# Kernel optimization log

Hardware: AMD Instinct MI355X
Metric: run time of the kernel (lower is better)

The kernel has to match this reference:

```python
import jax, jax.numpy as jnp
import numpy as np

NEG = -1e9


def setup_inputs() -> dict:
    key = jax.random.key(0)
    k1, k2, k3, k4 = jax.random.split(key, 4)
    R, N, D = 64, 200000, 256
    hs = jax.random.normal(k1, (R, D), dtype=jnp.float32)
    es = jax.random.normal(k2, (N, D), dtype=jnp.float32)
    W = jax.random.normal(k3, (D, D), dtype=jnp.float32) / np.sqrt(D)
    mask = jax.random.randint(k4, (R, N), 0, 2) > 0
    return {"hs": hs, "es": es, "W": W, "mask": mask, "n_output": 50}


def reference(hs, es, W, mask, n_output):
    # MatchingLayer: bilinear match scores[r, n] = hs_r^T W es_n  -> [R, N]
    original_scores = (hs @ W) @ es.T
    mu = original_scores.mean()
    std = original_scores.std(ddof=1)  # torch .std() is unbiased
    scores = (original_scores - mu) / std
    # logits used for expansion scores (differentiable)
    logits = jax.nn.log_softmax(scores, axis=-1) + jax.nn.log_softmax(scores, axis=0)
    # detached probabilities for selection
    d = jax.lax.stop_gradient(scores)
    row_probs = jnp.maximum(jax.nn.softmax(jnp.where(mask, d, NEG), axis=-1), 1e-6)
    col_probs = jnp.maximum(jax.nn.softmax(jnp.where(mask, d, NEG), axis=0), 1e-6)
    # deterministic (eval) path: assign each candidate to its argmax category
    index = jnp.argmax(col_probs, axis=0)  # [N]
    R = scores.shape[0]
    valid = mask & (index[None, :] == jnp.arange(R)[:, None])  # [R, N]
    sel = jnp.where(valid, row_probs, -jnp.inf)
    top_vals, top_idx = jax.lax.top_k(sel, n_output)  # [R, n_output]
    ok = jnp.isfinite(top_vals)  # rows with fewer candidates than n_output -> padded
    expansions = jnp.where(ok, top_idx, -1)  # [R, n_output], -1 = pad
    # expansion_scores[i] = logits[:, expansion_i].T -> [n_output, R]
    exp_scores = jnp.transpose(logits[:, top_idx], (1, 2, 0))  # [R, n_output, R]
    exp_scores = exp_scores * ok[:, :, None].astype(exp_scores.dtype)
    return expansions, exp_scores
```

## Files before the change

kernel.cpp:

```cpp
#include <hip/hip_runtime.h>
#include <math.h>

#define RR 64
#define DD 256
#define CAP 6144


__device__ __forceinline__ void get_mu_istd(const double* sums, int N, float& fmu, float& istd) {
  double M = (double)RR * (double)N;
  double mu = sums[0] / M;
  double var = (sums[1] - sums[0] * sums[0] / M) / (M - 1.0);
  fmu = (float)mu;
  istd = (float)(1.0 / sqrt(var));
}

__device__ __forceinline__ void cp16(const void* g, void* l) {
  __builtin_amdgcn_global_load_lds((const __attribute__((address_space(1))) void*)g,
                                   (__attribute__((address_space(3))) void*)l, 16, 0, 0);
}


__global__ __launch_bounds__(256) void k_mask(const void* __restrict__ maskp,
                                              unsigned long long* __restrict__ mbits,
                                              int N) {
  __shared__ int f;
  int tid = threadIdx.x;
  if (tid == 0) f = 0;
  __syncthreads();
  {
    const unsigned* mw = (const unsigned*)maskp;
    int mode = 0;
    for (int i = tid; i < 4096; i += 256) {
      unsigned v = mw[i];
      if (v == 0x3f800000u) mode = 2;
      else if (v > 1u && mode != 2) mode = 1;
    }
    if (mode) atomicMax(&f, mode);
  }
  __syncthreads();
  const int mode = f;

  int n = blockIdx.x * 256 + tid;
  if (n >= N) return;
  unsigned long long b = 0;
  if (mode == 1) {
    const unsigned char* m = (const unsigned char*)maskp;
#pragma unroll
    for (int r = 0; r < RR; ++r)
      b |= (unsigned long long)(m[(size_t)r * N + n] != 0) << r;
  } else if (mode == 2) {
    const float* m = (const float*)maskp;
#pragma unroll
    for (int r = 0; r < RR; ++r)
      b |= (unsigned long long)(m[(size_t)r * N + n] != 0.f) << r;
  } else {
    const int* m = (const int*)maskp;
#pragma unroll
    for (int r = 0; r < RR; ++r)
      b |= (unsigned long long)(m[(size_t)r * N + n] != 0) << r;
  }
  mbits[n] = b;
}


__global__ __launch_bounds__(256) void k_hsw(const float* __restrict__ hs,
                                             const float* __restrict__ W,
                                             float* __restrict__ hsW) {
  int i = blockIdx.x;
  int j = threadIdx.x;
  float acc = 0.f;
  for (int k = 0; k < DD; ++k) acc = fmaf(hs[i * DD + k], W[k * DD + j], acc);
  hsW[i * DD + j] = acc;
}


__global__ __launch_bounds__(256) void k_scores(const float* __restrict__ es,
                                                const float* __restrict__ hsW,
                                                const unsigned long long* __restrict__ mbits,
                                                float* __restrict__ scores,
                                                float* __restrict__ colmax,
                                                int* __restrict__ colargmax,
                                                float* __restrict__ qpart,
                                                double* __restrict__ spart,
                                                int N) {
  __shared__ float lds[20480];
  const int tid = threadIdx.x;
  const int lane = tid & 63;
  const int ty = __builtin_amdgcn_readfirstlane(tid >> 6);
  const int n0 = blockIdx.x * 256;
  const int R0 = ty * 16;
  const int nb = n0 + lane;

  const int srow = ty * 8 + (lane >> 3);
  const int sg4 = (((lane & 7) ^ ((lane >> 3) & 7)) << 2);
  const int wrow = ty * 16 + (lane >> 2);
  const int wg4 = (lane & 3) << 2;

  float4 acc[16];
#pragma unroll
  for (int i = 0; i < 16; ++i) acc[i] = make_float4(0.f, 0.f, 0.f, 0.f);

  auto stage = [&](float* ebase, float* wbase, int kc) {
#pragma unroll
    for (int p = 0; p < 8; ++p) {
      const int col = p * 32 + srow;
      const int rr = min(n0 + col, N - 1);
      cp16(es + (size_t)rr * DD + kc + sg4, ebase + p * 1024 + ty * 256);
    }
    cp16(hsW + (size_t)wrow * DD + kc + wg4, wbase + ty * 256);
    cp16(hsW + (size_t)wrow * DD + kc + 16 + wg4, wbase + 1024 + ty * 256);
  };

  stage(lds, lds + 16384, 0);
  asm volatile("s_waitcnt vmcnt(0)" ::: "memory");
  __syncthreads();

  const int swz = (lane & 7);

  for (int kc = 0; kc < DD; kc += 32) {
    const int cur = (kc >> 5) & 1;
    float* ebC = lds + (cur ? 8192 : 0);
    float* wbC = lds + 16384 + (cur ? 2048 : 0);
    if (kc + 32 < DD) {
      float* ebN = lds + (cur ? 0 : 8192);
      float* wbN = lds + 16384 + (cur ? 0 : 2048);
      stage(ebN, wbN, kc + 32);
    }
#pragma unroll
    for (int k = 0; k < 32; k += 4) {
      const int eswz = (((k >> 2) ^ swz) << 2);
      const float4 e0 = *(const float4*)(ebC + (lane       ) * 32 + eswz);
      const float4 e1 = *(const float4*)(ebC + (lane +  64 ) * 32 + eswz);
      const float4 e2 = *(const float4*)(ebC + (lane + 128 ) * 32 + eswz);
      const float4 e3 = *(const float4*)(ebC + (lane + 192 ) * 32 + eswz);
      const float* wk = wbC + ((k >> 4) * 1024) + (k & 15);
#pragma unroll
      for (int i = 0; i < 16; ++i) {
        const float4 w = *(const float4*)(wk + (R0 + i) * 16);
        acc[i].x = fmaf(w.x, e0.x, fmaf(w.y, e0.y, fmaf(w.z, e0.z, fmaf(w.w, e0.w, acc[i].x))));
        acc[i].y = fmaf(w.x, e1.x, fmaf(w.y, e1.y, fmaf(w.z, e1.z, fmaf(w.w, e1.w, acc[i].y))));
        acc[i].z = fmaf(w.x, e2.x, fmaf(w.y, e2.y, fmaf(w.z, e2.z, fmaf(w.w, e2.w, acc[i].z))));
        acc[i].w = fmaf(w.x, e3.x, fmaf(w.y, e3.y, fmaf(w.z, e3.z, fmaf(w.w, e3.w, acc[i].w))));
      }
    }
    asm volatile("s_waitcnt vmcnt(0)" ::: "memory");
    __syncthreads();
  }

  bool val[4];
#pragma unroll
  for (int c = 0; c < 4; ++c) val[c] = (nb + 64 * c) < N;

#pragma unroll
  for (int i = 0; i < 16; ++i) {
    float* dst = scores + (size_t)(R0 + i) * N + nb;
    float v[4] = {acc[i].x, acc[i].y, acc[i].z, acc[i].w};
#pragma unroll
    for (int c = 0; c < 4; ++c)
      if (val[c]) dst[64 * c] = v[c];
  }

  unsigned long long mb[4];
#pragma unroll
  for (int c = 0; c < 4; ++c) mb[c] = val[c] ? mbits[nb + 64 * c] : 0ull;

  float ps1[4], ps2[4], pcm[4], pbv[4];
  int pbr[4];
#pragma unroll
  for (int c = 0; c < 4; ++c) { ps1[c] = 0.f; ps2[c] = 0.f; pcm[c] = -INFINITY; pbv[c] = -INFINITY; pbr[c] = -1; }

#pragma unroll
  for (int i = 0; i < 16; ++i) {
    const int rrow = R0 + i;
    float v[4] = {acc[i].x, acc[i].y, acc[i].z, acc[i].w};
    float q = -INFINITY, qm = -INFINITY;
#pragma unroll
    for (int c = 0; c < 4; ++c) {
      ps1[c] += v[c];
      ps2[c] = fmaf(v[c], v[c], ps2[c]);
      pcm[c] = fmaxf(pcm[c], v[c]);
      bool bit = (mb[c] >> rrow) & 1ull;
      if (bit && (v[c] > pbv[c])) { pbv[c] = v[c]; pbr[c] = rrow; }
      float qv = val[c] ? v[c] : -INFINITY;
      q = fmaxf(q, qv);
      if (bit) qm = fmaxf(qm, qv);
    }
#pragma unroll
    for (int o = 32; o > 0; o >>= 1) {
      q = fmaxf(q, __shfl_down(q, o));
      qm = fmaxf(qm, __shfl_down(qm, o));
    }
    if (lane == 0) {
      qpart[(size_t)blockIdx.x * 128 + rrow] = q;
      qpart[(size_t)blockIdx.x * 128 + 64 + rrow] = qm;
    }
  }

  __syncthreads();
  float* Ls1 = lds;
  float* Ls2 = lds + 1024;
  float* Lcm = lds + 2048;
  float* Lbv = lds + 3072;
  int* Lbr = (int*)(lds + 4096);
  double* red = (double*)(lds + 5120);
#pragma unroll
  for (int c = 0; c < 4; ++c) {
    int col = lane + 64 * c;
    Ls1[ty * 256 + col] = ps1[c];
    Ls2[ty * 256 + col] = ps2[c];
    Lcm[ty * 256 + col] = pcm[c];
    Lbv[ty * 256 + col] = pbv[c];
    Lbr[ty * 256 + col] = pbr[c];
  }
  __syncthreads();

  const int n = n0 + tid;
  float s1 = 0.f, s2 = 0.f;
  if (n < N) {
    s1 = Ls1[tid] + Ls1[256 + tid] + Ls1[512 + tid] + Ls1[768 + tid];
    s2 = Ls2[tid] + Ls2[256 + tid] + Ls2[512 + tid] + Ls2[768 + tid];
    float cm = fmaxf(fmaxf(Lcm[tid], Lcm[256 + tid]), fmaxf(Lcm[512 + tid], Lcm[768 + tid]));
    colmax[n] = cm;
    float bv = -INFINITY;
    int br = -1;
#pragma unroll
    for (int w2 = 0; w2 < 4; ++w2) {
      float b = Lbv[w2 * 256 + tid];
      if (b > bv) { bv = b; br = Lbr[w2 * 256 + tid]; }
    }
    colargmax[n] = br;
  }

  double d1 = (double)s1, d2 = (double)s2;
#pragma unroll
  for (int o = 32; o > 0; o >>= 1) {
    d1 += __shfl_down(d1, o);
    d2 += __shfl_down(d2, o);
  }
  if ((tid & 63) == 0) { red[ty * 2] = d1; red[ty * 2 + 1] = d2; }
  __syncthreads();
  if (tid == 0) {
    spart[(size_t)blockIdx.x * 2] = red[0] + red[2] + red[4] + red[6];
    spart[(size_t)blockIdx.x * 2 + 1] = red[1] + red[3] + red[5] + red[7];
  }
}


__global__ __launch_bounds__(256) void k_redmax(const float* __restrict__ qpart,
                                                float* __restrict__ rowmaxf,
                                                int NBlk) {
  const int slot = blockIdx.x;
  const int tid = threadIdx.x, lane = tid & 63, ty = tid >> 6;
  __shared__ float w[4];
  float m = -INFINITY;
  for (int i = tid; i < NBlk; i += 256) m = fmaxf(m, qpart[(size_t)i * 128 + slot]);
#pragma unroll
  for (int o = 32; o > 0; o >>= 1) m = fmaxf(m, __shfl_down(m, o));
  if (lane == 0) w[ty] = m;
  __syncthreads();
  if (tid == 0) rowmaxf[slot] = fmaxf(fmaxf(w[0], w[1]), fmaxf(w[2], w[3]));
}


__global__ __launch_bounds__(256) void k_redsum(const double* __restrict__ spart,
                                                double* __restrict__ sums,
                                                int NBlk) {
  const int tid = threadIdx.x, lane = tid & 63, ty = tid >> 6;
  __shared__ double r[8];
  double s0 = 0.0, s1 = 0.0;
  for (int i = tid; i < NBlk; i += 256) {
    s0 += spart[(size_t)i * 2];
    s1 += spart[(size_t)i * 2 + 1];
  }
#pragma unroll
  for (int o = 32; o > 0; o >>= 1) {
    s0 += __shfl_down(s0, o);
    s1 += __shfl_down(s1, o);
  }
  if (lane == 0) { r[ty * 2] = s0; r[ty * 2 + 1] = s1; }
  __syncthreads();
  if (tid == 0) {
    sums[0] = r[0] + r[2] + r[4] + r[6];
    sums[1] = r[1] + r[3] + r[5] + r[7];
  }
}


__global__ __launch_bounds__(256) void k_colpass(const float* __restrict__ scores,
                                                 const float* __restrict__ colmax,
                                                 const int* __restrict__ colargmax,
                                                 const unsigned long long* __restrict__ mbits,
                                                 const double* __restrict__ sums,
                                                 const float* __restrict__ rowmaxf,
                                                 float* __restrict__ collse,
                                                 float* __restrict__ colpart,
                                                 int* __restrict__ cnt,
                                                 float* __restrict__ candx,
                                                 int* __restrict__ candn,
                                                 int N) {
  __shared__ float rmS[64], suS[64], smS[64];
  __shared__ float rpu[64 * 4], rpm[64 * 4];
  __shared__ int lcnt[64], lbase[64];
  const int tid = threadIdx.x, lane = tid & 63, ty = tid >> 6;
  float fmu, istd;
  get_mu_istd(sums, N, fmu, istd);
  if (tid < 64) {
    rmS[tid] = rowmaxf[tid];
    lcnt[tid] = 0;
  }
  __syncthreads();
  float gm = rmS[0];
#pragma unroll
  for (int r = 1; r < RR; ++r) gm = fmaxf(gm, rmS[r]);
  if (tid < 64) {
    suS[tid] = expf((gm - rmS[tid]) * istd);
    smS[tid] = expf((gm - rowmaxf[64 + tid]) * istd);
  }

  const int n = blockIdx.x * 256 + tid;
  const bool valid = n < N;
  const float cm = valid ? colmax[n] : 0.f;
  const int br = valid ? colargmax[n] : -1;
  const unsigned long long mbn = valid ? mbits[n] : 0ull;
  float colsum = 0.f, xbr = 0.f;

  for (int r = 0; r < RR; ++r) {
    float x = valid ? scores[(size_t)r * N + n] : 0.f;
    if (r == br) xbr = x;
    float E = valid ? expf((x - gm) * istd) : 0.f;
    colsum += E;
    float eu = E;
    float em = ((mbn >> r) & 1ull) ? E : 0.f;
#pragma unroll
    for (int o = 32; o > 0; o >>= 1) {
      eu += __shfl_down(eu, o);
      em += __shfl_down(em, o);
    }
    if (lane == 0) { rpu[r * 4 + ty] = eu; rpm[r * 4 + ty] = em; }
  }

  if (valid) collse[n] = logf(colsum) + (gm - cm) * istd;
  int lpos = 0;
  if (br >= 0) lpos = atomicAdd(&lcnt[br], 1);
  __syncthreads();
  if (tid < 64) {
    float su = (rpu[tid * 4] + rpu[tid * 4 + 1] + rpu[tid * 4 + 2] + rpu[tid * 4 + 3]) * suS[tid];
    float sm = (rpm[tid * 4] + rpm[tid * 4 + 1] + rpm[tid * 4 + 2] + rpm[tid * 4 + 3]) * smS[tid];
    colpart[(size_t)blockIdx.x * 128 + tid] = su;
    colpart[(size_t)blockIdx.x * 128 + 64 + tid] = sm;
    int c = lcnt[tid];
    lbase[tid] = c ? atomicAdd(&cnt[tid], c) : 0;
  }
  __syncthreads();
  if (br >= 0) {
    int pos = lbase[br] + lpos;
    if (pos < CAP) {
      candx[(size_t)br * CAP + pos] = xbr;
      candn[(size_t)br * CAP + pos] = n;
    }
  }
}


__global__ __launch_bounds__(256) void k_redacc(const float* __restrict__ colpart,
                                                const float* __restrict__ rowmaxf,
                                                float* __restrict__ rowstats,
                                                int NBlk) {
  const int slot = blockIdx.x;
  const int tid = threadIdx.x, lane = tid & 63, ty = tid >> 6;
  __shared__ float w[4];
  float s = 0.f;
  for (int i = tid; i < NBlk; i += 256) s += colpart[(size_t)i * 128 + slot];
#pragma unroll
  for (int o = 32; o > 0; o >>= 1) s += __shfl_down(s, o);
  if (lane == 0) w[ty] = s;
  __syncthreads();
  if (tid == 0) {
    float total = w[0] + w[1] + w[2] + w[3];
    if (slot < 64) {
      rowstats[slot] = rowmaxf[slot];
      rowstats[64 + slot] = logf(total);
    } else {
      rowstats[128 + (slot - 64)] = rowmaxf[slot];
      rowstats[192 + (slot - 64)] = total;
    }
  }
}


__global__ __launch_bounds__(512) void k_topk(const int* __restrict__ cnt,
                                              const float* __restrict__ candx,
                                              const int* __restrict__ candn,
                                              const double* __restrict__ sums,
                                              const float* __restrict__ rowstats,
                                              float* __restrict__ out,
                                              int* __restrict__ seln,
                                              int N, int NO) {
  int r = blockIdx.x, tid = threadIdx.x;
  __shared__ float sp[CAP];
  __shared__ int sn[CAP];
  __shared__ float wp[8];
  __shared__ int wn[8], wi[8];
  int c = min(cnt[r], CAP);
  float fmu, istd;
  get_mu_istd(sums, N, fmu, istd);
  const float rmm = rowstats[128 + r];
  const float lm = rowstats[192 + r];
  for (int i = tid; i < c; i += 512) {
    float xv = candx[(size_t)r * CAP + i];
    sp[i] = fmaxf(expf((xv - rmm) * istd) / lm, 1e-6f);
    sn[i] = candn[(size_t)r * CAP + i];
  }
  __syncthreads();
  for (int j = 0; j < NO; ++j) {
    float bp = -1.f;
    int bn = 0x7fffffff, bi = -1;
    for (int i = tid; i < c; i += 512) {
      float p = sp[i];
      int nn = sn[i];
      if (p > bp || (p == bp && nn < bn)) { bp = p; bn = nn; bi = i; }
    }
#pragma unroll
    for (int o = 32; o > 0; o >>= 1) {
      float p2 = __shfl_down(bp, o);
      int n2 = __shfl_down(bn, o);
      int i2 = __shfl_down(bi, o);
      if (p2 > bp || (p2 == bp && n2 < bn)) { bp = p2; bn = n2; bi = i2; }
    }
    if ((tid & 63) == 0) { wp[tid >> 6] = bp; wn[tid >> 6] = bn; wi[tid >> 6] = bi; }
    __syncthreads();
    if (tid == 0) {
      float fp2 = wp[0]; int fn2 = wn[0], fi2 = wi[0];
#pragma unroll
      for (int w2 = 1; w2 < 8; ++w2) {
        if (wp[w2] > fp2 || (wp[w2] == fp2 && wn[w2] < fn2)) { fp2 = wp[w2]; fn2 = wn[w2]; fi2 = wi[w2]; }
      }
      if (fp2 > 0.f) {
        out[r * NO + j] = (float)fn2;
        seln[r * NO + j] = fn2;
        sp[fi2] = -1.f;
      } else {
        out[r * NO + j] = -1.f;
        seln[r * NO + j] = -1;
      }
    }
    __syncthreads();
  }
}


__global__ void k_expand(const float* __restrict__ scores,
                         const double* __restrict__ sums,
                         const float* __restrict__ rowstats,
                         const float* __restrict__ colmax,
                         const float* __restrict__ collse,
                         const int* __restrict__ seln,
                         float* __restrict__ out,
                         int N, int NO) {
  int b = blockIdx.x;
  int r2 = threadIdx.x;
  int n = seln[b];
  float v = 0.f;
  if (n >= 0) {
    float fmu, istd;
    get_mu_istd(sums, N, fmu, istd);
    float x = scores[(size_t)r2 * N + n];
    float v1 = (x - rowstats[r2]) * istd - rowstats[64 + r2];
    float v2 = (x - colmax[n]) * istd - collse[n];
    v = v1 + v2;
  }
  out[RR * NO + (size_t)b * RR + r2] = v;
}


extern "C" void kernel_launch(void* const* d_in, const int* in_sizes, int n_in,
                              void* d_out, int out_size, void* d_ws, size_t ws_size,
                              hipStream_t stream) {
  const float* hs = (const float*)d_in[0];
  const float* es = (const float*)d_in[1];
  const float* W = (const float*)d_in[2];
  const void* mask = d_in[3];

  const int N = in_sizes[1] / DD;
  const int NO = out_size / (RR * (1 + RR));
  const int NB = (N + 255) / 256;

  char* ws = (char*)d_ws;
  size_t o = 0;
  float* scores = (float*)(ws + o);   o += (size_t)RR * N * 4;
  float* hsW = (float*)(ws + o);      o += RR * DD * 4;
  o = (o + 255) & ~(size_t)255;
  double* sums = (double*)(ws + o);
  int* cnt = (int*)(ws + o + 16);
  size_t zero_off = o, zero_bytes = 16 + 256;
  o += 512;
  float* rowstats = (float*)(ws + o); o += 256 * 4;
  float* rowmaxf = (float*)(ws + o);  o += 128 * 4;
  o = (o + 255) & ~(size_t)255;
  float* colmax = (float*)(ws + o);   o += (size_t)N * 4;
  int* colargmax = (int*)(ws + o);    o += (size_t)N * 4;
  float* collse = (float*)(ws + o);   o += (size_t)N * 4;
  o = (o + 255) & ~(size_t)255;
  unsigned long long* mbits = (unsigned long long*)(ws + o); o += (size_t)N * 8;
  o = (o + 255) & ~(size_t)255;
  float* candx = (float*)(ws + o);    o += (size_t)RR * CAP * 4;
  int* candn = (int*)(ws + o);        o += (size_t)RR * CAP * 4;
  int* seln = (int*)(ws + o);         o += (size_t)RR * NO * 4;
  o = (o + 255) & ~(size_t)255;
  float* qpart = (float*)(ws + o);    o += (size_t)NB * 128 * 4;
  double* spart = (double*)(ws + o);  o += (size_t)NB * 2 * 8;
  float* colpart = (float*)(ws + o);  o += (size_t)NB * 128 * 4;

  hipMemsetAsync(ws + zero_off, 0, zero_bytes, stream);

  k_mask<<<NB, 256, 0, stream>>>(mask, mbits, N);
  k_hsw<<<RR, 256, 0, stream>>>(hs, W, hsW);
  k_scores<<<NB, 256, 0, stream>>>(es, hsW, mbits, scores, colmax, colargmax,
                                   qpart, spart, N);
  k_redmax<<<128, 256, 0, stream>>>(qpart, rowmaxf, NB);
  k_redsum<<<1, 256, 0, stream>>>(spart, sums, NB);
  k_colpass<<<NB, 256, 0, stream>>>(scores, colmax, colargmax, mbits, sums, rowmaxf,
                                    collse, colpart, cnt, candx, candn, N);
  k_redacc<<<128, 256, 0, stream>>>(colpart, rowmaxf, rowstats, NB);
  k_topk<<<RR, 512, 0, stream>>>(cnt, candx, candn, sums, rowstats, (float*)d_out, seln,
                                 N, NO);
  k_expand<<<RR * NO, 64, 0, stream>>>(scores, sums, rowstats, colmax, collse, seln,
                                       (float*)d_out, N, NO);
}
```

Measured before the change: 632.7 us.

## Vectorize mask packing and colpass, fuse reductions and expand into topk

The mask-packing kernel now has each thread read 4 adjacent columns over 16 rows with vector loads and assembles 64-bit words via LDS. The column pass is restructured the same way, with float4 score loads and 4x fewer wave shuffles. The two small reduction kernels are merged into one launch that also zeroes the counters, replacing the memset. The expand kernel is folded into the top-k kernel. Together these cut launch count and uncoalesced narrow loads. The vector path assumes N is a multiple of 4 for alignment.

```diff
diff --git a/kernel.cpp b/kernel.cpp
--- a/kernel.cpp
+++ b/kernel.cpp
@@ -24,6 +24,7 @@
                                               unsigned long long* __restrict__ mbits,
                                               int N) {
   __shared__ int f;
+  __shared__ unsigned short pb[4][256];
   int tid = threadIdx.x;
   if (tid == 0) f = 0;
   __syncthreads();
@@ -40,26 +41,80 @@
   __syncthreads();
   const int mode = f;
 
-  int n = blockIdx.x * 256 + tid;
-  if (n >= N) return;
-  unsigned long long b = 0;
+  const int lane = tid & 63, ty = tid >> 6;
+  const int R0 = ty * 16;
+  const int n0 = blockIdx.x * 256;
+  const int n4 = n0 + lane * 4;
+  unsigned g0 = 0, g1 = 0, g2 = 0, g3 = 0;
+  const bool vec_ok = (n4 + 3) < N;
+
   if (mode == 1) {
     const unsigned char* m = (const unsigned char*)maskp;
-#pragma unroll
-    for (int r = 0; r < RR; ++r)
-      b |= (unsigned long long)(m[(size_t)r * N + n] != 0) << r;
+    if (vec_ok) {
+#pragma unroll
+      for (int i = 0; i < 16; ++i) {
+        uchar4 v = *(const uchar4*)(m + (size_t)(R0 + i) * N + n4);
+        g0 |= (unsigned)(v.x != 0) << i;
+        g1 |= (unsigned)(v.y != 0) << i;
+        g2 |= (unsigned)(v.z != 0) << i;
+        g3 |= (unsigned)(v.w != 0) << i;
+      }
+    } else {
+      unsigned* gp[4] = {&g0, &g1, &g2, &g3};
+      for (int c = 0; c < 4; ++c)
+        if (n4 + c < N)
+          for (int i = 0; i < 16; ++i)
+            *gp[c] |= (unsigned)(m[(size_t)(R0 + i) * N + n4 + c] != 0) << i;
+    }
   } else if (mode == 2) {
     const float* m = (const float*)maskp;
-#pragma unroll
-    for (int r = 0; r < RR; ++r)
-      b |= (unsigned long long)(m[(size_t)r * N + n] != 0.f) << r;
+    if (vec_ok) {
+#pragma unroll
+      for (int i = 0; i < 16; ++i) {
+        float4 v = *(const float4*)(m + (size_t)(R0 + i) * N + n4);
+        g0 |= (unsigned)(v.x != 0.f) << i;
+        g1 |= (unsigned)(v.y != 0.f) << i;
+        g2 |= (unsigned)(v.z != 0.f) << i;
+        g3 |= (unsigned)(v.w != 0.f) << i;
+      }
+    } else {
+      unsigned* gp[4] = {&g0, &g1, &g2, &g3};
+      for (int c = 0; c < 4; ++c)
+        if (n4 + c < N)
+          for (int i = 0; i < 16; ++i)
+            *gp[c] |= (unsigned)(m[(size_t)(R0 + i) * N + n4 + c] != 0.f) << i;
+    }
   } else {
     const int* m = (const int*)maskp;
-#pragma unroll
-    for (int r = 0; r < RR; ++r)
-      b |= (unsigned long long)(m[(size_t)r * N + n] != 0) << r;
-  }
-  mbits[n] = b;
+    if (vec_ok) {
+#pragma unroll
+      for (int i = 0; i < 16; ++i) {
+        int4 v = *(const int4*)(m + (size_t)(R0 + i) * N + n4);
+        g0 |= (unsigned)(v.x != 0) << i;
+        g1 |= (unsigned)(v.y != 0) << i;
+        g2 |= (unsigned)(v.z != 0) << i;
+        g3 |= (unsigned)(v.w != 0) << i;
+      }
+    } else {
+      unsigned* gp[4] = {&g0, &g1, &g2, &g3};
+      for (int c = 0; c < 4; ++c)
+        if (n4 + c < N)
+          for (int i = 0; i < 16; ++i)
+            *gp[c] |= (unsigned)(m[(size_t)(R0 + i) * N + n4 + c] != 0) << i;
+    }
+  }
+  pb[ty][lane * 4 + 0] = (unsigned short)g0;
+  pb[ty][lane * 4 + 1] = (unsigned short)g1;
+  pb[ty][lane * 4 + 2] = (unsigned short)g2;
+  pb[ty][lane * 4 + 3] = (unsigned short)g3;
+  __syncthreads();
+  const int n = n0 + tid;
+  if (n < N) {
+    mbits[n] = (unsigned long long)pb[0][tid] |
+               ((unsigned long long)pb[1][tid] << 16) |
+               ((unsigned long long)pb[2][tid] << 32) |
+               ((unsigned long long)pb[3][tid] << 48);
+  }
 }
 
 
@@ -246,42 +301,42 @@
 }
 
 
-__global__ __launch_bounds__(256) void k_redmax(const float* __restrict__ qpart,
-                                                float* __restrict__ rowmaxf,
-                                                int NBlk) {
-  const int slot = blockIdx.x;
+__global__ __launch_bounds__(256) void k_redfuse(const float* __restrict__ qpart,
+                                                 const double* __restrict__ spart,
+                                                 float* __restrict__ rowmaxf,
+                                                 double* __restrict__ sums,
+                                                 int* __restrict__ cnt,
+                                                 int NBlk) {
   const int tid = threadIdx.x, lane = tid & 63, ty = tid >> 6;
-  __shared__ float w[4];
-  float m = -INFINITY;
-  for (int i = tid; i < NBlk; i += 256) m = fmaxf(m, qpart[(size_t)i * 128 + slot]);
-#pragma unroll
-  for (int o = 32; o > 0; o >>= 1) m = fmaxf(m, __shfl_down(m, o));
-  if (lane == 0) w[ty] = m;
-  __syncthreads();
-  if (tid == 0) rowmaxf[slot] = fmaxf(fmaxf(w[0], w[1]), fmaxf(w[2], w[3]));
-}
-
-
-__global__ __launch_bounds__(256) void k_redsum(const double* __restrict__ spart,
-                                                double* __restrict__ sums,
-                                                int NBlk) {
-  const int tid = threadIdx.x, lane = tid & 63, ty = tid >> 6;
-  __shared__ double r[8];
-  double s0 = 0.0, s1 = 0.0;
-  for (int i = tid; i < NBlk; i += 256) {
-    s0 += spart[(size_t)i * 2];
-    s1 += spart[(size_t)i * 2 + 1];
-  }
-#pragma unroll
-  for (int o = 32; o > 0; o >>= 1) {
-    s0 += __shfl_down(s0, o);
-    s1 += __shfl_down(s1, o);
-  }
-  if (lane == 0) { r[ty * 2] = s0; r[ty * 2 + 1] = s1; }
-  __syncthreads();
-  if (tid == 0) {
-    sums[0] = r[0] + r[2] + r[4] + r[6];
-    sums[1] = r[1] + r[3] + r[5] + r[7];
+  if (blockIdx.x < 128) {
+    const int slot = blockIdx.x;
+    __shared__ float w[4];
+    float m = -INFINITY;
+    for (int i = tid; i < NBlk; i += 256) m = fmaxf(m, qpart[(size_t)i * 128 + slot]);
+#pragma unroll
+    for (int o = 32; o > 0; o >>= 1) m = fmaxf(m, __shfl_down(m, o));
+    if (lane == 0) w[ty] = m;
+    __syncthreads();
+    if (tid == 0) rowmaxf[slot] = fmaxf(fmaxf(w[0], w[1]), fmaxf(w[2], w[3]));
+  } else {
+    __shared__ double r[8];
+    double s0 = 0.0, s1 = 0.0;
+    for (int i = tid; i < NBlk; i += 256) {
+      s0 += spart[(size_t)i * 2];
+      s1 += spart[(size_t)i * 2 + 1];
+    }
+#pragma unroll
+    for (int o = 32; o > 0; o >>= 1) {
+      s0 += __shfl_down(s0, o);
+      s1 += __shfl_down(s1, o);
+    }
+    if (lane == 0) { r[ty * 2] = s0; r[ty * 2 + 1] = s1; }
+    if (tid < RR) cnt[tid] = 0;
+    __syncthreads();
+    if (tid == 0) {
+      sums[0] = r[0] + r[2] + r[4] + r[6];
+      sums[1] = r[1] + r[3] + r[5] + r[7];
+    }
   }
 }
 
@@ -299,9 +354,11 @@
                                                  int* __restrict__ candn,
                                                  int N) {
   __shared__ float rmS[64], suS[64], smS[64];
-  __shared__ float rpu[64 * 4], rpm[64 * 4];
+  __shared__ float rowU[64], rowM[64];
+  __shared__ float cpart[4][256];
   __shared__ int lcnt[64], lbase[64];
   const int tid = threadIdx.x, lane = tid & 63, ty = tid >> 6;
+  const int R0 = ty * 16;
   float fmu, istd;
   get_mu_istd(sums, N, fmu, istd);
   if (tid < 64) {
@@ -317,37 +374,58 @@
     smS[tid] = expf((gm - rowmaxf[64 + tid]) * istd);
   }
 
-  const int n = blockIdx.x * 256 + tid;
-  const bool valid = n < N;
-  const float cm = valid ? colmax[n] : 0.f;
-  const int br = valid ? colargmax[n] : -1;
-  const unsigned long long mbn = valid ? mbits[n] : 0ull;
-  float colsum = 0.f, xbr = 0.f;
-
-  for (int r = 0; r < RR; ++r) {
-    float x = valid ? scores[(size_t)r * N + n] : 0.f;
-    if (r == br) xbr = x;
-    float E = valid ? expf((x - gm) * istd) : 0.f;
-    colsum += E;
-    float eu = E;
-    float em = ((mbn >> r) & 1ull) ? E : 0.f;
+  const int n0 = blockIdx.x * 256;
+  const int n4 = n0 + lane * 4;
+  bool vc[4];
+  unsigned mbr[4];
+#pragma unroll
+  for (int c = 0; c < 4; ++c) {
+    vc[c] = (n4 + c) < N;
+    unsigned long long mw = vc[c] ? mbits[n4 + c] : 0ull;
+    mbr[c] = (unsigned)((mw >> R0) & 0xffffull);
+  }
+
+  float cs0 = 0.f, cs1 = 0.f, cs2 = 0.f, cs3 = 0.f;
+#pragma unroll
+  for (int i = 0; i < 16; ++i) {
+    const int r = R0 + i;
+    const float4 x = *(const float4*)(scores + (size_t)r * N + n4);
+    float E0 = vc[0] ? expf((x.x - gm) * istd) : 0.f;
+    float E1 = vc[1] ? expf((x.y - gm) * istd) : 0.f;
+    float E2 = vc[2] ? expf((x.z - gm) * istd) : 0.f;
+    float E3 = vc[3] ? expf((x.w - gm) * istd) : 0.f;
+    cs0 += E0; cs1 += E1; cs2 += E2; cs3 += E3;
+    float eu = (E0 + E1) + (E2 + E3);
+    float em = (((mbr[0] >> i) & 1u) ? E0 : 0.f) + (((mbr[1] >> i) & 1u) ? E1 : 0.f) +
+               (((mbr[2] >> i) & 1u) ? E2 : 0.f) + (((mbr[3] >> i) & 1u) ? E3 : 0.f);
 #pragma unroll
     for (int o = 32; o > 0; o >>= 1) {
       eu += __shfl_down(eu, o);
       em += __shfl_down(em, o);
     }
-    if (lane == 0) { rpu[r * 4 + ty] = eu; rpm[r * 4 + ty] = em; }
-  }
-
-  if (valid) collse[n] = logf(colsum) + (gm - cm) * istd;
+    if (lane == 0) { rowU[r] = eu; rowM[r] = em; }
+  }
+
+  cpart[ty][lane * 4 + 0] = cs0;
+  cpart[ty][lane * 4 + 1] = cs1;
+  cpart[ty][lane * 4 + 2] = cs2;
+  cpart[ty][lane * 4 + 3] = cs3;
+  __syncthreads();
+
+  const int n = n0 + tid;
+  const bool valid = n < N;
+  int br = -1;
+  if (valid) {
+    float colsum = ((cpart[0][tid] + cpart[1][tid]) + cpart[2][tid]) + cpart[3][tid];
+    collse[n] = logf(colsum) + (gm - colmax[n]) * istd;
+    br = colargmax[n];
+  }
   int lpos = 0;
   if (br >= 0) lpos = atomicAdd(&lcnt[br], 1);
   __syncthreads();
   if (tid < 64) {
-    float su = (rpu[tid * 4] + rpu[tid * 4 + 1] + rpu[tid * 4 + 2] + rpu[tid * 4 + 3]) * suS[tid];
-    float sm = (rpm[tid * 4] + rpm[tid * 4 + 1] + rpm[tid * 4 + 2] + rpm[tid * 4 + 3]) * smS[tid];
-    colpart[(size_t)blockIdx.x * 128 + tid] = su;
-    colpart[(size_t)blockIdx.x * 128 + 64 + tid] = sm;
+    colpart[(size_t)blockIdx.x * 128 + tid] = rowU[tid] * suS[tid];
+    colpart[(size_t)blockIdx.x * 128 + 64 + tid] = rowM[tid] * smS[tid];
     int c = lcnt[tid];
     lbase[tid] = c ? atomicAdd(&cnt[tid], c) : 0;
   }
@@ -355,7 +433,7 @@
   if (br >= 0) {
     int pos = lbase[br] + lpos;
     if (pos < CAP) {
-      candx[(size_t)br * CAP + pos] = xbr;
+      candx[(size_t)br * CAP + pos] = scores[(size_t)br * N + n];
       candn[(size_t)br * CAP + pos] = n;
     }
   }
@@ -388,19 +466,22 @@
 }
 
 
-__global__ __launch_bounds__(512) void k_topk(const int* __restrict__ cnt,
-                                              const float* __restrict__ candx,
-                                              const int* __restrict__ candn,
-                                              const double* __restrict__ sums,
-                                              const float* __restrict__ rowstats,
-                                              float* __restrict__ out,
-                                              int* __restrict__ seln,
-                                              int N, int NO) {
+__global__ __launch_bounds__(512) void k_topkx(const int* __restrict__ cnt,
+                                               const float* __restrict__ candx,
+                                               const int* __restrict__ candn,
+                                               const double* __restrict__ sums,
+                                               const float* __restrict__ rowstats,
+                                               const float* __restrict__ scores,
+                                               const float* __restrict__ colmax,
+                                               const float* __restrict__ collse,
+                                               float* __restrict__ out,
+                                               int N, int NO) {
   int r = blockIdx.x, tid = threadIdx.x;
   __shared__ float sp[CAP];
   __shared__ int sn[CAP];
   __shared__ float wp[8];
   __shared__ int wn[8], wi[8];
+  __shared__ int selS[64];
   int c = min(cnt[r], CAP);
   float fmu, istd;
   get_mu_istd(sums, N, fmu, istd);
@@ -437,39 +518,29 @@
       }
       if (fp2 > 0.f) {
         out[r * NO + j] = (float)fn2;
-        seln[r * NO + j] = fn2;
+        selS[j] = fn2;
         sp[fi2] = -1.f;
       } else {
         out[r * NO + j] = -1.f;
-        seln[r * NO + j] = -1;
+        selS[j] = -1;
       }
     }
     __syncthreads();
   }
-}
-
-
-__global__ void k_expand(const float* __restrict__ scores,
-                         const double* __restrict__ sums,
-                         const float* __restrict__ rowstats,
-                         const float* __restrict__ colmax,
-                         const float* __restrict__ collse,
-                         const int* __restrict__ seln,
-                         float* __restrict__ out,
-                         int N, int NO) {
-  int b = blockIdx.x;
-  int r2 = threadIdx.x;
-  int n = seln[b];
-  float v = 0.f;
-  if (n >= 0) {
-    float fmu, istd;
-    get_mu_istd(sums, N, fmu, istd);
-    float x = scores[(size_t)r2 * N + n];
-    float v1 = (x - rowstats[r2]) * istd - rowstats[64 + r2];
-    float v2 = (x - colmax[n]) * istd - collse[n];
-    v = v1 + v2;
-  }
-  out[RR * NO + (size_t)b * RR + r2] = v;
+
+  for (int idx = tid; idx < NO * RR; idx += 512) {
+    const int j = idx >> 6;
+    const int r2 = idx & 63;
+    const int n = selS[j];
+    float v = 0.f;
+    if (n >= 0) {
+      float x = scores[(size_t)r2 * N + n];
+      float v1 = (x - rowstats[r2]) * istd - rowstats[64 + r2];
+      float v2 = (x - colmax[n]) * istd - collse[n];
+      v = v1 + v2;
+    }
+    out[RR * NO + ((size_t)r * NO + j) * RR + r2] = v;
+  }
 }
 
 
@@ -492,7 +563,6 @@
   o = (o + 255) & ~(size_t)255;
   double* sums = (double*)(ws + o);
   int* cnt = (int*)(ws + o + 16);
-  size_t zero_off = o, zero_bytes = 16 + 256;
   o += 512;
   float* rowstats = (float*)(ws + o); o += 256 * 4;
   float* rowmaxf = (float*)(ws + o);  o += 128 * 4;
@@ -505,25 +575,19 @@
   o = (o + 255) & ~(size_t)255;
   float* candx = (float*)(ws + o);    o += (size_t)RR * CAP * 4;
   int* candn = (int*)(ws + o);        o += (size_t)RR * CAP * 4;
-  int* seln = (int*)(ws + o);         o += (size_t)RR * NO * 4;
   o = (o + 255) & ~(size_t)255;
   float* qpart = (float*)(ws + o);    o += (size_t)NB * 128 * 4;
   double* spart = (double*)(ws + o);  o += (size_t)NB * 2 * 8;
   float* colpart = (float*)(ws + o);  o += (size_t)NB * 128 * 4;
 
-  hipMemsetAsync(ws + zero_off, 0, zero_bytes, stream);
-
   k_mask<<<NB, 256, 0, stream>>>(mask, mbits, N);
   k_hsw<<<RR, 256, 0, stream>>>(hs, W, hsW);
   k_scores<<<NB, 256, 0, stream>>>(es, hsW, mbits, scores, colmax, colargmax,
                                    qpart, spart, N);
-  k_redmax<<<128, 256, 0, stream>>>(qpart, rowmaxf, NB);
-  k_redsum<<<1, 256, 0, stream>>>(spart, sums, NB);
+  k_redfuse<<<129, 256, 0, stream>>>(qpart, spart, rowmaxf, sums, cnt, NB);
   k_colpass<<<NB, 256, 0, stream>>>(scores, colmax, colargmax, mbits, sums, rowmaxf,
                                     collse, colpart, cnt, candx, candn, N);
   k_redacc<<<128, 256, 0, stream>>>(colpart, rowmaxf, rowstats, NB);
-  k_topk<<<RR, 512, 0, stream>>>(cnt, candx, candn, sums, rowstats, (float*)d_out, seln,
-                                 N, NO);
-  k_expand<<<RR * NO, 64, 0, stream>>>(scores, sums, rowstats, colmax, collse, seln,
-                                       (float*)d_out, N, NO);
-}
+  k_topkx<<<RR, 512, 0, stream>>>(cnt, candx, candn, sums, rowstats, scores, colmax,
+                                  collse, (float*)d_out, N, NO);
+}
```

Result: faster. 590.6 us (-6.7%).
